# Performance work log

Measured on AMD Instinct MI355X. Metric: run time of the kernel, lower is better.

## Reference

```python
import jax, jax.numpy as jnp
import numpy as np

N = 50000
E = 400000
IN_CH = 16
HID = 64
HEADS = 4
NEG_SLOPE = 0.2


def setup_inputs() -> dict:
    key = jax.random.key(0)
    ks = jax.random.split(key, 12)
    x_dyn = jax.random.normal(ks[0], (N, IN_CH), dtype=jnp.float32)
    edge_index = jax.random.randint(ks[1], (2, E), 0, N, dtype=jnp.int64)
    s = 0.1
    # conv1: heads=HEADS, out=HID, concat=False
    W1 = jax.random.normal(ks[2], (IN_CH, HEADS * HID), dtype=jnp.float32) * s
    att_src1 = jax.random.normal(ks[3], (HEADS, HID), dtype=jnp.float32) * s
    att_dst1 = jax.random.normal(ks[4], (HEADS, HID), dtype=jnp.float32) * s
    b1 = jnp.zeros((HID,), dtype=jnp.float32)
    # conv2: heads=1, out=HID
    W2 = jax.random.normal(ks[5], (HID, 1 * HID), dtype=jnp.float32) * s
    att_src2 = jax.random.normal(ks[6], (1, HID), dtype=jnp.float32) * s
    att_dst2 = jax.random.normal(ks[7], (1, HID), dtype=jnp.float32) * s
    b2 = jnp.zeros((HID,), dtype=jnp.float32)
    return {"x_dyn": x_dyn, "edge_index": edge_index,
            "W1": W1, "att_src1": att_src1, "att_dst1": att_dst1, "b1": b1,
            "W2": W2, "att_src2": att_src2, "att_dst2": att_dst2, "b2": b2}


def gat_conv(x, src, dst, W, att_src, att_dst, bias, heads, out_ch):
    n = x.shape[0]
    h = (x @ W).reshape(n, heads, out_ch)                 # [N,H,C]
    a_src = jnp.sum(h * att_src[None], axis=-1)           # [N,H]
    a_dst = jnp.sum(h * att_dst[None], axis=-1)           # [N,H]
    e = jax.nn.leaky_relu(a_src[src] + a_dst[dst], NEG_SLOPE)  # [E,H]
    # softmax over incoming edges per destination node (stable)
    emax = jax.ops.segment_max(e, dst, num_segments=n)    # [N,H]
    ex = jnp.exp(e - emax[dst])
    denom = jax.ops.segment_sum(ex, dst, num_segments=n)  # [N,H]
    alpha = ex / (denom[dst] + 1e-16)                     # [E,H]
    msg = h[src] * alpha[:, :, None]                      # [E,H,C]
    out = jax.ops.segment_sum(msg, dst, num_segments=n)   # [N,H,C]
    return jnp.mean(out, axis=1) + bias                   # concat=False -> mean over heads


def reference(x_dyn, edge_index, W1, att_src1, att_dst1, b1, W2, att_src2, att_dst2, b2):
    n = x_dyn.shape[0]
    # PyG GATConv default: add self-loops
    loop = jnp.arange(n, dtype=edge_index.dtype)
    src = jnp.concatenate([edge_index[0], loop])
    dst = jnp.concatenate([edge_index[1], loop])
    h = jax.nn.elu(gat_conv(x_dyn, src, dst, W1, att_src1, att_dst1, b1, HEADS, HID))
    h = jax.nn.elu(gat_conv(h, src, dst, W2, att_src2, att_dst2, b2, 1, HID))
    return h
```

## Files before the change

kernel.cpp:

```cpp
#include <hip/hip_runtime.h>
#include <math.h>


#define CAP 40

typedef __attribute__((ext_vector_type(8))) short s8v;
typedef __attribute__((ext_vector_type(4))) float f4v;

__device__ __forceinline__ float leaky02(float x) { return x > 0.f ? x : 0.2f * x; }
__device__ __forceinline__ float eluf(float x) { return x > 0.f ? x : expm1f(x); }
__device__ __forceinline__ unsigned short f2bf(float f) {
    unsigned u = __float_as_uint(f);
    u += 0x7FFFu + ((u >> 16) & 1u);
    return (unsigned short)(u >> 16);
}
__device__ __forceinline__ float bf2f(unsigned short h) {
    return __uint_as_float((unsigned)h << 16);
}


__global__ void k_deg_prep(const int* __restrict__ src, const int* __restrict__ dst,
                           int* __restrict__ deg, int* __restrict__ csr_src, int e_cnt,
                           const float* __restrict__ x, const float* __restrict__ W1,
                           const float* __restrict__ W2,
                           const float* __restrict__ attS, const float* __restrict__ attD,
                           unsigned short* __restrict__ xb,
                           unsigned short* __restrict__ w1catT,
                           unsigned short* __restrict__ w2tb,
                           float* __restrict__ a_src1, float* __restrict__ a_dst1,
                           int n16, int n4) {
    __shared__ float wS[64], wD[64];
    int t = threadIdx.x;
    int i = blockIdx.x * 256 + t;
    if (i < 4096) {
        int c = i >> 6, k = i & 63;
        w2tb[c * 64 + k] = f2bf(W2[k * 64 + c]);
        int r = i & 63;
        int h = r >> 4, k2 = r & 15;
        w1catT[c * 64 + r] = f2bf(0.25f * W1[k2 * 256 + h * 64 + c]);
    }
    if (i < n16) xb[i] = f2bf(x[i]);
    if (i < e_cnt) {
        int d = dst[i];
        int r = atomicAdd(&deg[d], 1);
        csr_src[d * CAP + r] = src[i];
    }
    if ((int)blockIdx.x * 256 < n4) {
        if (t < 64) {
            int h = t >> 4, k = t & 15;
            float s = 0.f, d = 0.f;
            for (int c = 0; c < 64; ++c) {
                float w = W1[k * 256 + h * 64 + c];
                s += w * attS[h * 64 + c];
                d += w * attD[h * 64 + c];
            }
            wS[t] = s; wD[t] = d;
        }
        __syncthreads();
        if (i < n4) {
            int n = i >> 2, h = i & 3;
            const float4* xr = (const float4*)(x + (size_t)n * 16);
            const float* ws = wS + h * 16;
            const float* wd = wD + h * 16;
            float s = 0.f, d = 0.f;
#pragma unroll
            for (int q = 0; q < 4; ++q) {
                float4 xv = xr[q];
                s += xv.x * ws[4 * q] + xv.y * ws[4 * q + 1] + xv.z * ws[4 * q + 2] + xv.w * ws[4 * q + 3];
                d += xv.x * wd[4 * q] + xv.y * wd[4 * q + 1] + xv.z * wd[4 * q + 2] + xv.w * wd[4 * q + 3];
            }
            a_src1[i] = s;
            a_dst1[i] = d;
        }
    }
}

__global__ void __launch_bounds__(256)
k45_agg_mlp(const int* __restrict__ deg, const int* __restrict__ csr_src,
            const unsigned short* __restrict__ xb,
            const float* __restrict__ a_src1, const float* __restrict__ a_dst1,
            const unsigned short* __restrict__ w1catT, const unsigned short* __restrict__ w2tb,
            const float* __restrict__ b1, const float* __restrict__ attS2,
            const float* __restrict__ attD2, unsigned short* __restrict__ h2b,
            float* __restrict__ a_src2, float* __restrict__ a_dst2, int n_nodes) {
    __shared__ unsigned short xaggS[16 * 72];
    __shared__ unsigned short x2s[16 * 72];
    __shared__ int   sS[4][16];
    __shared__ float eS[4][64];
    __shared__ float psS[4][16], pdS[4][16];
    const int wave = threadIdx.x >> 6, lane = threadIdx.x & 63;
    const int head = lane >> 4, k = lane & 15;
    const int h4 = lane & 3, eidx = lane >> 2;
    const int base = blockIdx.x * 16;
#pragma unroll 1
    for (int r = 0; r < 4; ++r) {
        int n = base + wave * 4 + r;
        float agg = 0.f, den = 1e-16f;
        if (n < n_nodes) {
            int beg = n * CAP, end = beg + deg[n];
            float se = expf(leaky02(a_src1[n * 4 + head] + a_dst1[n * 4 + head]));
            den += se;
            agg = se * bf2f(xb[(size_t)n * 16 + k]);
            float adn = a_dst1[n * 4 + h4];
            for (int cb = beg; cb < end; cb += 16) {
                int m = end - cb; if (m > 16) m = 16;
                if (eidx < m) {
                    int s = csr_src[cb + eidx];
                    if (h4 == 0) sS[wave][eidx] = s;
                    eS[wave][lane] = expf(leaky02(a_src1[s * 4 + h4] + adn));
                }
                int i = 0;
                for (; i + 8 <= m; i += 8) {
                    int s0 = sS[wave][i];     float e0 = eS[wave][4 * i + head];
                    int s1 = sS[wave][i + 1]; float e1 = eS[wave][4 * (i + 1) + head];
                    int s2 = sS[wave][i + 2]; float e2 = eS[wave][4 * (i + 2) + head];
                    int s3 = sS[wave][i + 3]; float e3 = eS[wave][4 * (i + 3) + head];
                    int s4 = sS[wave][i + 4]; float e4 = eS[wave][4 * (i + 4) + head];
                    int s5 = sS[wave][i + 5]; float e5 = eS[wave][4 * (i + 5) + head];
                    int s6 = sS[wave][i + 6]; float e6 = eS[wave][4 * (i + 6) + head];
                    int s7 = sS[wave][i + 7]; float e7 = eS[wave][4 * (i + 7) + head];
                    float v0 = bf2f(xb[(size_t)s0 * 16 + k]);
                    float v1 = bf2f(xb[(size_t)s1 * 16 + k]);
                    float v2 = bf2f(xb[(size_t)s2 * 16 + k]);
                    float v3 = bf2f(xb[(size_t)s3 * 16 + k]);
                    float v4 = bf2f(xb[(size_t)s4 * 16 + k]);
                    float v5 = bf2f(xb[(size_t)s5 * 16 + k]);
                    float v6 = bf2f(xb[(size_t)s6 * 16 + k]);
                    float v7 = bf2f(xb[(size_t)s7 * 16 + k]);
                    agg += e0 * v0 + e1 * v1 + e2 * v2 + e3 * v3
                         + e4 * v4 + e5 * v5 + e6 * v6 + e7 * v7;
                    den += e0 + e1 + e2 + e3 + e4 + e5 + e6 + e7;
                }
                for (; i < m; ++i) {
                    int s = sS[wave][i];
                    float eh = eS[wave][4 * i + head];
                    agg += eh * bf2f(xb[(size_t)s * 16 + k]);
                    den += eh;
                }
            }
        }
        xaggS[(wave * 4 + r) * 72 + lane] = f2bf(agg / den);
    }
    __syncthreads();
    const int quad = lane >> 4, l16 = lane & 15;
    const int c = wave * 16 + l16;
    const s8v a0 = *(const s8v*)(xaggS + l16 * 72 + quad * 8);
    const s8v a1f = *(const s8v*)(xaggS + l16 * 72 + 32 + quad * 8);
    const s8v c0 = *(const s8v*)(w1catT + c * 64 + quad * 8);
    const s8v c1 = *(const s8v*)(w1catT + c * 64 + 32 + quad * 8);
    f4v acc = {0.f, 0.f, 0.f, 0.f};
    acc = __builtin_amdgcn_mfma_f32_16x16x32_bf16(a0, c0, acc, 0, 0, 0);
    acc = __builtin_amdgcn_mfma_f32_16x16x32_bf16(a1f, c1, acc, 0, 0, 0);
    float b1c = b1[c];
#pragma unroll
    for (int r = 0; r < 4; ++r)
        x2s[(quad * 4 + r) * 72 + c] = f2bf(eluf(acc[r] + b1c));
    __syncthreads();
    const s8v b0 = *(const s8v*)(w2tb + c * 64 + quad * 8);
    const s8v b1v = *(const s8v*)(w2tb + c * 64 + 32 + quad * 8);
    const s8v a2_0 = *(const s8v*)(x2s + l16 * 72 + quad * 8);
    const s8v a2_1 = *(const s8v*)(x2s + l16 * 72 + 32 + quad * 8);
    f4v acc2 = {0.f, 0.f, 0.f, 0.f};
    acc2 = __builtin_amdgcn_mfma_f32_16x16x32_bf16(a2_0, b0, acc2, 0, 0, 0);
    acc2 = __builtin_amdgcn_mfma_f32_16x16x32_bf16(a2_1, b1v, acc2, 0, 0, 0);
    const float attS_c = attS2[c], attD_c = attD2[c];
    float pS[4], pD[4];
#pragma unroll
    for (int r = 0; r < 4; ++r) {
        int node = base + quad * 4 + r;
        if (node < n_nodes) h2b[(size_t)node * 64 + c] = f2bf(acc2[r]);
        pS[r] = acc2[r] * attS_c;
        pD[r] = acc2[r] * attD_c;
    }
#pragma unroll
    for (int mask = 1; mask < 16; mask <<= 1) {
#pragma unroll
        for (int r = 0; r < 4; ++r) {
            pS[r] += __shfl_xor(pS[r], mask, 64);
            pD[r] += __shfl_xor(pD[r], mask, 64);
        }
    }
    if (l16 == 0) {
#pragma unroll
        for (int r = 0; r < 4; ++r) {
            psS[wave][quad * 4 + r] = pS[r];
            pdS[wave][quad * 4 + r] = pD[r];
        }
    }
    __syncthreads();
    if (threadIdx.x < 16) {
        int node = base + threadIdx.x;
        if (node < n_nodes) {
            a_src2[node] = psS[0][threadIdx.x] + psS[1][threadIdx.x] +
                           psS[2][threadIdx.x] + psS[3][threadIdx.x];
            a_dst2[node] = pdS[0][threadIdx.x] + pdS[1][threadIdx.x] +
                           pdS[2][threadIdx.x] + pdS[3][threadIdx.x];
        }
    }
}


__global__ void __launch_bounds__(256, 6)
k8_agg2(const int* __restrict__ deg, const int* __restrict__ csr_src,
        const unsigned short* __restrict__ h2b,
        const float* __restrict__ a_src2, const float* __restrict__ a_dst2,
        const float* __restrict__ b2, float* __restrict__ out, int n_nodes) {
    __shared__ int   sS[4][64];
    __shared__ float eS[4][64];
    const int wave = threadIdx.x >> 6, lane = threadIdx.x & 63;
    const int g = lane >> 4, l16 = lane & 15;
    const float4 b2v = ((const float4*)b2)[l16];
    for (int n = blockIdx.x * 4 + wave; n < n_nodes; n += gridDim.x * 4) {
        int beg = n * CAP, end = beg + deg[n];
        float adn = a_dst2[n];
        float se = expf(leaky02(a_src2[n] + adn));
        ushort4 qs = ((const ushort4*)(h2b + (size_t)n * 64))[l16];
        float w0 = (g == 0) ? se : 0.f;
        float a0 = w0 * bf2f(qs.x), a1 = w0 * bf2f(qs.y);
        float a2 = w0 * bf2f(qs.z), a3 = w0 * bf2f(qs.w);
        float den = w0;
        for (int base = beg; base < end; base += 64) {
            int m = end - base; if (m > 64) m = 64;
            if (lane < m) {
                int s = csr_src[base + lane];
                sS[wave][lane] = s;
                eS[wave][lane] = expf(leaky02(a_src2[s] + adn));
            }
            int i = g;
            for (; i + 12 < m; i += 16) {
                int s0 = sS[wave][i];
                int s1 = sS[wave][i + 4];
                int s2 = sS[wave][i + 8];
                int s3 = sS[wave][i + 12];
                ushort4 q0 = ((const ushort4*)(h2b + (size_t)s0 * 64))[l16];
                ushort4 q1 = ((const ushort4*)(h2b + (size_t)s1 * 64))[l16];
                ushort4 q2 = ((const ushort4*)(h2b + (size_t)s2 * 64))[l16];
                ushort4 q3 = ((const ushort4*)(h2b + (size_t)s3 * 64))[l16];
                float e0 = eS[wave][i];
                float e1 = eS[wave][i + 4];
                float e2 = eS[wave][i + 8];
                float e3 = eS[wave][i + 12];
                a0 += e0 * bf2f(q0.x) + e1 * bf2f(q1.x) + e2 * bf2f(q2.x) + e3 * bf2f(q3.x);
                a1 += e0 * bf2f(q0.y) + e1 * bf2f(q1.y) + e2 * bf2f(q2.y) + e3 * bf2f(q3.y);
                a2 += e0 * bf2f(q0.z) + e1 * bf2f(q1.z) + e2 * bf2f(q2.z) + e3 * bf2f(q3.z);
                a3 += e0 * bf2f(q0.w) + e1 * bf2f(q1.w) + e2 * bf2f(q2.w) + e3 * bf2f(q3.w);
                den += e0 + e1 + e2 + e3;
            }
            for (; i < m; i += 4) {
                int s = sS[wave][i];
                float eh = eS[wave][i];
                ushort4 q = ((const ushort4*)(h2b + (size_t)s * 64))[l16];
                a0 += eh * bf2f(q.x); a1 += eh * bf2f(q.y);
                a2 += eh * bf2f(q.z); a3 += eh * bf2f(q.w);
                den += eh;
            }
        }
        a0 += __shfl_xor(a0, 16, 64); a0 += __shfl_xor(a0, 32, 64);
        a1 += __shfl_xor(a1, 16, 64); a1 += __shfl_xor(a1, 32, 64);
        a2 += __shfl_xor(a2, 16, 64); a2 += __shfl_xor(a2, 32, 64);
        a3 += __shfl_xor(a3, 16, 64); a3 += __shfl_xor(a3, 32, 64);
        den += __shfl_xor(den, 16, 64); den += __shfl_xor(den, 32, 64);
        if (lane < 16) {
            float inv = 1.f / (den + 1e-16f);
            float4 ov;
            ov.x = eluf(a0 * inv + b2v.x);
            ov.y = eluf(a1 * inv + b2v.y);
            ov.z = eluf(a2 * inv + b2v.z);
            ov.w = eluf(a3 * inv + b2v.w);
            ((float4*)(out + (size_t)n * 64))[l16] = ov;
        }
    }
}

extern "C" void kernel_launch(void* const* d_in, const int* in_sizes, int n_in,
                              void* d_out, int out_size, void* d_ws, size_t ws_size,
                              hipStream_t stream) {
    const float* x   = (const float*)d_in[0];
    const int*   ei  = (const int*)d_in[1];
    const float* W1  = (const float*)d_in[2];
    const float* as1 = (const float*)d_in[3];
    const float* ad1 = (const float*)d_in[4];
    const float* b1  = (const float*)d_in[5];
    const float* W2  = (const float*)d_in[6];
    const float* as2 = (const float*)d_in[7];
    const float* ad2 = (const float*)d_in[8];
    const float* b2  = (const float*)d_in[9];
    float* out = (float*)d_out;

    const int n = in_sizes[0] / 16;
    const int e = in_sizes[1] / 2;
    const int* src = ei;
    const int* dst = ei + e;

    float* ws = (float*)d_ws;
    size_t o = 0;
    unsigned short* xb     = (unsigned short*)(ws + o); o += (size_t)n * 8;
    unsigned short* w2tb   = (unsigned short*)(ws + o); o += 2048;
    unsigned short* w1catT = (unsigned short*)(ws + o); o += 2048;
    float*  a_src1  = ws + o; o += (size_t)n * 4;
    float*  a_dst1  = ws + o; o += (size_t)n * 4;
    unsigned short* h2b = (unsigned short*)(ws + o); o += (size_t)n * 32;
    float*  a_src2  = ws + o; o += (size_t)n;
    float*  a_dst2  = ws + o; o += (size_t)n;
    int*    csr_src = (int*)(ws + o); o += (size_t)n * CAP;
    int*    deg     = (int*)(ws + o); o += (size_t)n;

    hipMemsetAsync(deg, 0, (size_t)n * sizeof(int), stream);

    const int prep_threads = (n * 16 > e) ? n * 16 : e;
    k_deg_prep<<<(prep_threads + 255) / 256, 256, 0, stream>>>(
        src, dst, deg, csr_src, e, x, W1, W2, as1, ad1, xb, w1catT, w2tb,
        a_src1, a_dst1, n * 16, n * 4);

    k45_agg_mlp<<<(n + 15) / 16, 256, 0, stream>>>(deg, csr_src, xb,
                                                   a_src1, a_dst1, w1catT, w2tb, b1,
                                                   as2, ad2, h2b, a_src2, a_dst2, n);

    k8_agg2<<<(n + 3) / 4, 256, 0, stream>>>(deg, csr_src, h2b, a_src2, a_dst2, b2, out, n);
}
```

Before: 160.4 us.

## Add low-degree fast path and fixed-unroll gather batching in GAT aggregation kernels

The layer-1 aggregation kernel gains a fast path for the case where all four nodes a wave handles have degree at most 16. That path loads their CSR sources and attention exponents for all four nodes at once, so the gathers for several nodes are in flight together instead of being serialized per node. The layer-2 aggregation replaces its chunked loop with a fixed eight-slot unrolled gather covering 32 neighbors (zero-padded, reading index 0 for empty slots), plus a remainder loop for higher degrees. It also lowers the k8_agg2 launch-bounds occupancy hint from 6 to 4 to allow more registers. Degree is clamped to CAP everywhere, which guards against CSR overflow. The cost is extra register pressure and some wasted padded gathers for low-degree nodes.

```diff
diff --git a/kernel.cpp b/kernel.cpp
--- a/kernel.cpp
+++ b/kernel.cpp
@@ -41,9 +41,10 @@
     }
     if (i < n16) xb[i] = f2bf(x[i]);
     if (i < e_cnt) {
+        int sv = src[i];
         int d = dst[i];
         int r = atomicAdd(&deg[d], 1);
-        csr_src[d * CAP + r] = src[i];
+        if (r < CAP) csr_src[d * CAP + r] = sv;
     }
     if ((int)blockIdx.x * 256 < n4) {
         if (t < 64) {
@@ -85,61 +86,130 @@
             float* __restrict__ a_src2, float* __restrict__ a_dst2, int n_nodes) {
     __shared__ unsigned short xaggS[16 * 72];
     __shared__ unsigned short x2s[16 * 72];
-    __shared__ int   sS[4][16];
-    __shared__ float eS[4][64];
+    __shared__ int   sS[4][4][16];
+    __shared__ float eSf[4][4][64];
     __shared__ float psS[4][16], pdS[4][16];
     const int wave = threadIdx.x >> 6, lane = threadIdx.x & 63;
     const int head = lane >> 4, k = lane & 15;
     const int h4 = lane & 3, eidx = lane >> 2;
     const int base = blockIdx.x * 16;
+
+    int nn[4], mm[4];
+    bool val[4];
+#pragma unroll
+    for (int r = 0; r < 4; ++r) {
+        nn[r] = base + wave * 4 + r;
+        val[r] = nn[r] < n_nodes;
+        mm[r] = val[r] ? deg[nn[r]] : 0;
+        if (mm[r] > CAP) mm[r] = CAP;
+    }
+    bool fast = (mm[0] <= 16) && (mm[1] <= 16) && (mm[2] <= 16) && (mm[3] <= 16);
+    if (fast) {
+        int sreg[4];
+#pragma unroll
+        for (int r = 0; r < 4; ++r)
+            sreg[r] = (eidx < mm[r]) ? csr_src[nn[r] * CAP + eidx] : 0;
+        float adn[4], selS[4], selD[4], xself[4];
+#pragma unroll
+        for (int r = 0; r < 4; ++r) {
+            adn[r]   = val[r] ? a_dst1[nn[r] * 4 + h4] : 0.f;
+            selS[r]  = val[r] ? a_src1[nn[r] * 4 + head] : 0.f;
+            selD[r]  = val[r] ? a_dst1[nn[r] * 4 + head] : 0.f;
+            xself[r] = val[r] ? bf2f(xb[(size_t)nn[r] * 16 + k]) : 0.f;
+        }
+        float ereg[4];
+#pragma unroll
+        for (int r = 0; r < 4; ++r) {
+            float as = (eidx < mm[r]) ? a_src1[(size_t)sreg[r] * 4 + h4] : 0.f;
+            ereg[r] = (eidx < mm[r]) ? expf(leaky02(as + adn[r])) : 0.f;
+        }
+#pragma unroll
+        for (int r = 0; r < 4; ++r) {
+            if (h4 == 0) sS[wave][r][eidx] = sreg[r];
+            eSf[wave][r][lane] = ereg[r];
+        }
+#pragma unroll
+        for (int r = 0; r < 4; ++r) {
+            float se = val[r] ? expf(leaky02(selS[r] + selD[r])) : 0.f;
+            float agg = se * xself[r], den = 1e-16f + se;
+            if (mm[r] > 0) {
+#pragma unroll
+                for (int blk = 0; blk < 16; blk += 8) {
+                    if (blk < mm[r]) {
+                        int s0 = sS[wave][r][blk];     float e0 = eSf[wave][r][4 * blk + head];
+                        int s1 = sS[wave][r][blk + 1]; float e1 = eSf[wave][r][4 * (blk + 1) + head];
+                        int s2 = sS[wave][r][blk + 2]; float e2 = eSf[wave][r][4 * (blk + 2) + head];
+                        int s3 = sS[wave][r][blk + 3]; float e3 = eSf[wave][r][4 * (blk + 3) + head];
+                        int s4 = sS[wave][r][blk + 4]; float e4 = eSf[wave][r][4 * (blk + 4) + head];
+                        int s5 = sS[wave][r][blk + 5]; float e5 = eSf[wave][r][4 * (blk + 5) + head];
+                        int s6 = sS[wave][r][blk + 6]; float e6 = eSf[wave][r][4 * (blk + 6) + head];
+                        int s7 = sS[wave][r][blk + 7]; float e7 = eSf[wave][r][4 * (blk + 7) + head];
+                        float v0 = bf2f(xb[(size_t)s0 * 16 + k]);
+                        float v1 = bf2f(xb[(size_t)s1 * 16 + k]);
+                        float v2 = bf2f(xb[(size_t)s2 * 16 + k]);
+                        float v3 = bf2f(xb[(size_t)s3 * 16 + k]);
+                        float v4 = bf2f(xb[(size_t)s4 * 16 + k]);
+                        float v5 = bf2f(xb[(size_t)s5 * 16 + k]);
+                        float v6 = bf2f(xb[(size_t)s6 * 16 + k]);
+                        float v7 = bf2f(xb[(size_t)s7 * 16 + k]);
+                        agg += e0 * v0 + e1 * v1 + e2 * v2 + e3 * v3
+                             + e4 * v4 + e5 * v5 + e6 * v6 + e7 * v7;
+                        den += e0 + e1 + e2 + e3 + e4 + e5 + e6 + e7;
+                    }
+                }
+            }
+            xaggS[(wave * 4 + r) * 72 + lane] = f2bf(agg / den);
+        }
+    } else {
 #pragma unroll 1
-    for (int r = 0; r < 4; ++r) {
-        int n = base + wave * 4 + r;
-        float agg = 0.f, den = 1e-16f;
-        if (n < n_nodes) {
-            int beg = n * CAP, end = beg + deg[n];
-            float se = expf(leaky02(a_src1[n * 4 + head] + a_dst1[n * 4 + head]));
-            den += se;
-            agg = se * bf2f(xb[(size_t)n * 16 + k]);
-            float adn = a_dst1[n * 4 + h4];
-            for (int cb = beg; cb < end; cb += 16) {
-                int m = end - cb; if (m > 16) m = 16;
-                if (eidx < m) {
-                    int s = csr_src[cb + eidx];
-                    if (h4 == 0) sS[wave][eidx] = s;
-                    eS[wave][lane] = expf(leaky02(a_src1[s * 4 + h4] + adn));
+        for (int r = 0; r < 4; ++r) {
+            int n = nn[r];
+            float agg = 0.f, den = 1e-16f;
+            if (val[r]) {
+                int beg = n * CAP, end = beg + mm[r];
+                float se = expf(leaky02(a_src1[n * 4 + head] + a_dst1[n * 4 + head]));
+                den += se;
+                agg = se * bf2f(xb[(size_t)n * 16 + k]);
+                float adn = a_dst1[n * 4 + h4];
+                for (int cb = beg; cb < end; cb += 16) {
+                    int m = end - cb; if (m > 16) m = 16;
+                    if (eidx < m) {
+                        int s = csr_src[cb + eidx];
+                        if (h4 == 0) sS[wave][0][eidx] = s;
+                        eSf[wave][0][lane] = expf(leaky02(a_src1[s * 4 + h4] + adn));
+                    }
+                    int i = 0;
+                    for (; i + 8 <= m; i += 8) {
+                        int s0 = sS[wave][0][i];     float e0 = eSf[wave][0][4 * i + head];
+                        int s1 = sS[wave][0][i + 1]; float e1 = eSf[wave][0][4 * (i + 1) + head];
+                        int s2 = sS[wave][0][i + 2]; float e2 = eSf[wave][0][4 * (i + 2) + head];
+                        int s3 = sS[wave][0][i + 3]; float e3 = eSf[wave][0][4 * (i + 3) + head];
+                        int s4 = sS[wave][0][i + 4]; float e4 = eSf[wave][0][4 * (i + 4) + head];
+                        int s5 = sS[wave][0][i + 5]; float e5 = eSf[wave][0][4 * (i + 5) + head];
+                        int s6 = sS[wave][0][i + 6]; float e6 = eSf[wave][0][4 * (i + 6) + head];
+                        int s7 = sS[wave][0][i + 7]; float e7 = eSf[wave][0][4 * (i + 7) + head];
+                        float v0 = bf2f(xb[(size_t)s0 * 16 + k]);
+                        float v1 = bf2f(xb[(size_t)s1 * 16 + k]);
+                        float v2 = bf2f(xb[(size_t)s2 * 16 + k]);
+                        float v3 = bf2f(xb[(size_t)s3 * 16 + k]);
+                        float v4 = bf2f(xb[(size_t)s4 * 16 + k]);
+                        float v5 = bf2f(xb[(size_t)s5 * 16 + k]);
+                        float v6 = bf2f(xb[(size_t)s6 * 16 + k]);
+                        float v7 = bf2f(xb[(size_t)s7 * 16 + k]);
+                        agg += e0 * v0 + e1 * v1 + e2 * v2 + e3 * v3
+                             + e4 * v4 + e5 * v5 + e6 * v6 + e7 * v7;
+                        den += e0 + e1 + e2 + e3 + e4 + e5 + e6 + e7;
+                    }
+                    for (; i < m; ++i) {
+                        int s = sS[wave][0][i];
+                        float eh = eSf[wave][0][4 * i + head];
+                        agg += eh * bf2f(xb[(size_t)s * 16 + k]);
+                        den += eh;
+                    }
                 }
-                int i = 0;
-                for (; i + 8 <= m; i += 8) {
-                    int s0 = sS[wave][i];     float e0 = eS[wave][4 * i + head];
-                    int s1 = sS[wave][i + 1]; float e1 = eS[wave][4 * (i + 1) + head];
-                    int s2 = sS[wave][i + 2]; float e2 = eS[wave][4 * (i + 2) + head];
-                    int s3 = sS[wave][i + 3]; float e3 = eS[wave][4 * (i + 3) + head];
-                    int s4 = sS[wave][i + 4]; float e4 = eS[wave][4 * (i + 4) + head];
-                    int s5 = sS[wave][i + 5]; float e5 = eS[wave][4 * (i + 5) + head];
-                    int s6 = sS[wave][i + 6]; float e6 = eS[wave][4 * (i + 6) + head];
-                    int s7 = sS[wave][i + 7]; float e7 = eS[wave][4 * (i + 7) + head];
-                    float v0 = bf2f(xb[(size_t)s0 * 16 + k]);
-                    float v1 = bf2f(xb[(size_t)s1 * 16 + k]);
-                    float v2 = bf2f(xb[(size_t)s2 * 16 + k]);
-                    float v3 = bf2f(xb[(size_t)s3 * 16 + k]);
-                    float v4 = bf2f(xb[(size_t)s4 * 16 + k]);
-                    float v5 = bf2f(xb[(size_t)s5 * 16 + k]);
-                    float v6 = bf2f(xb[(size_t)s6 * 16 + k]);
-                    float v7 = bf2f(xb[(size_t)s7 * 16 + k]);
-                    agg += e0 * v0 + e1 * v1 + e2 * v2 + e3 * v3
-                         + e4 * v4 + e5 * v5 + e6 * v6 + e7 * v7;
-                    den += e0 + e1 + e2 + e3 + e4 + e5 + e6 + e7;
-                }
-                for (; i < m; ++i) {
-                    int s = sS[wave][i];
-                    float eh = eS[wave][4 * i + head];
-                    agg += eh * bf2f(xb[(size_t)s * 16 + k]);
-                    den += eh;
-                }
-            }
-        }
-        xaggS[(wave * 4 + r) * 72 + lane] = f2bf(agg / den);
+            }
+            xaggS[(wave * 4 + r) * 72 + lane] = f2bf(agg / den);
+        }
     }
     __syncthreads();
     const int quad = lane >> 4, l16 = lane & 15;
@@ -200,7 +270,7 @@
 }
 
 
-__global__ void __launch_bounds__(256, 6)
+__global__ void __launch_bounds__(256, 4)
 k8_agg2(const int* __restrict__ deg, const int* __restrict__ csr_src,
         const unsigned short* __restrict__ h2b,
         const float* __restrict__ a_src2, const float* __restrict__ a_dst2,
@@ -211,44 +281,39 @@
     const int g = lane >> 4, l16 = lane & 15;
     const float4 b2v = ((const float4*)b2)[l16];
     for (int n = blockIdx.x * 4 + wave; n < n_nodes; n += gridDim.x * 4) {
-        int beg = n * CAP, end = beg + deg[n];
+        int m = deg[n]; if (m > CAP) m = CAP;
         float adn = a_dst2[n];
-        float se = expf(leaky02(a_src2[n] + adn));
+        float asn = a_src2[n];
         ushort4 qs = ((const ushort4*)(h2b + (size_t)n * 64))[l16];
+        int s_l = (lane < m) ? csr_src[n * CAP + lane] : 0;
+        float e_l = (lane < m) ? expf(leaky02(a_src2[s_l] + adn)) : 0.f;
+        sS[wave][lane] = s_l;
+        eS[wave][lane] = e_l;
+        float se = expf(leaky02(asn + adn));
         float w0 = (g == 0) ? se : 0.f;
         float a0 = w0 * bf2f(qs.x), a1 = w0 * bf2f(qs.y);
         float a2 = w0 * bf2f(qs.z), a3 = w0 * bf2f(qs.w);
         float den = w0;
-        for (int base = beg; base < end; base += 64) {
-            int m = end - base; if (m > 64) m = 64;
-            if (lane < m) {
-                int s = csr_src[base + lane];
-                sS[wave][lane] = s;
-                eS[wave][lane] = expf(leaky02(a_src2[s] + adn));
-            }
-            int i = g;
-            for (; i + 12 < m; i += 16) {
-                int s0 = sS[wave][i];
-                int s1 = sS[wave][i + 4];
-                int s2 = sS[wave][i + 8];
-                int s3 = sS[wave][i + 12];
-                ushort4 q0 = ((const ushort4*)(h2b + (size_t)s0 * 64))[l16];
-                ushort4 q1 = ((const ushort4*)(h2b + (size_t)s1 * 64))[l16];
-                ushort4 q2 = ((const ushort4*)(h2b + (size_t)s2 * 64))[l16];
-                ushort4 q3 = ((const ushort4*)(h2b + (size_t)s3 * 64))[l16];
-                float e0 = eS[wave][i];
-                float e1 = eS[wave][i + 4];
-                float e2 = eS[wave][i + 8];
-                float e3 = eS[wave][i + 12];
-                a0 += e0 * bf2f(q0.x) + e1 * bf2f(q1.x) + e2 * bf2f(q2.x) + e3 * bf2f(q3.x);
-                a1 += e0 * bf2f(q0.y) + e1 * bf2f(q1.y) + e2 * bf2f(q2.y) + e3 * bf2f(q3.y);
-                a2 += e0 * bf2f(q0.z) + e1 * bf2f(q1.z) + e2 * bf2f(q2.z) + e3 * bf2f(q3.z);
-                a3 += e0 * bf2f(q0.w) + e1 * bf2f(q1.w) + e2 * bf2f(q2.w) + e3 * bf2f(q3.w);
-                den += e0 + e1 + e2 + e3;
-            }
-            for (; i < m; i += 4) {
-                int s = sS[wave][i];
-                float eh = eS[wave][i];
+        int sj[8]; float ej[8]; ushort4 qj[8];
+#pragma unroll
+        for (int j = 0; j < 8; ++j) {
+            int slot = g + 4 * j;
+            sj[j] = sS[wave][slot];
+            ej[j] = eS[wave][slot];
+            qj[j] = ((const ushort4*)(h2b + (size_t)sj[j] * 64))[l16];
+        }
+#pragma unroll
+        for (int j = 0; j < 8; ++j) {
+            a0 += ej[j] * bf2f(qj[j].x);
+            a1 += ej[j] * bf2f(qj[j].y);
+            a2 += ej[j] * bf2f(qj[j].z);
+            a3 += ej[j] * bf2f(qj[j].w);
+            den += ej[j];
+        }
+        if (m > 32) {
+            for (int slot = g + 32; slot < m; slot += 4) {
+                int s = sS[wave][slot];
+                float eh = eS[wave][slot];
                 ushort4 q = ((const ushort4*)(h2b + (size_t)s * 64))[l16];
                 a0 += eh * bf2f(q.x); a1 += eh * bf2f(q.y);
                 a2 += eh * bf2f(q.z); a3 += eh * bf2f(q.w);
```

New measurement: 157.0 us. 2.1% less time.
